# Performance work log

Measured on AMD Instinct MI355X. Metric: run time of the kernel, lower is better.

## Reference

```python
import jax, jax.numpy as jnp
import numpy as np

D_MODEL = 1024
N_HEADS = 16
D_K = D_MODEL // N_HEADS  # 64
ROPE_BASE = 10000.0
MASK_FILL = -1e9


def _rope_cos_sin(seq_len, d_k, dtype):
    # inv_freq over even dims, freqs = outer(t, inv_freq): [S, d_k//2]
    inv_freq = 1.0 / (ROPE_BASE ** (jnp.arange(0, d_k, 2, dtype=jnp.float32) / d_k))
    freqs = jnp.arange(seq_len, dtype=jnp.float32)[:, None] * inv_freq[None, :]
    # broadcast to full d_k (rotate_half convention: same freq for x1 and x2 halves)
    cos = jnp.concatenate([jnp.cos(freqs), jnp.cos(freqs)], axis=-1).astype(dtype)
    sin = jnp.concatenate([jnp.sin(freqs), jnp.sin(freqs)], axis=-1).astype(dtype)
    return cos, sin  # each [S, d_k]


def _apply_rope(x, cos, sin):
    # x: [B, H, S, d_k]; rotate_half: (x1, x2) -> (-x2, x1)
    x1, x2 = jnp.split(x, 2, axis=-1)
    rot = jnp.concatenate([-x2, x1], axis=-1)
    return x * cos[None, None] + rot * sin[None, None]


def setup_inputs() -> dict:
    key = jax.random.key(0)
    kx, kqkv, ko = jax.random.split(key, 3)
    x = jax.random.normal(kx, (1, 4096, D_MODEL), dtype=jnp.float32)
    # nn.Linear weight shape [out, in]; y = x @ W.T
    s = 1.0 / np.sqrt(D_MODEL)
    W_qkv = jax.random.uniform(kqkv, (3 * D_MODEL, D_MODEL), jnp.float32, -s, s)
    W_o = jax.random.uniform(ko, (D_MODEL, D_MODEL), jnp.float32, -s, s)
    return {"x": x, "W_qkv": W_qkv, "W_o": W_o}


def reference(x, W_qkv, W_o):
    B, S, _ = x.shape
    qkv = jnp.einsum("bsd,ed->bse", x, W_qkv)  # [B, S, 3*d_model]
    Q, K, V = jnp.split(qkv, 3, axis=-1)
    # [B, S, H, d_k] -> [B, H, S, d_k]
    reshape = lambda t: t.reshape(B, S, N_HEADS, D_K).transpose(0, 2, 1, 3)
    Q, K, V = reshape(Q), reshape(K), reshape(V)
    cos, sin = _rope_cos_sin(S, D_K, x.dtype)
    Q = _apply_rope(Q, cos, sin)
    K = _apply_rope(K, cos, sin)
    scores = jnp.einsum("bhqd,bhkd->bhqk", Q, K) / jnp.sqrt(jnp.asarray(D_K, x.dtype))
    causal = jnp.tril(jnp.ones((S, S), dtype=bool))
    scores = jnp.where(causal[None, None], scores, jnp.asarray(MASK_FILL, x.dtype))
    attn = jax.nn.softmax(scores, axis=-1)  # dropout inactive at inference
    out = jnp.einsum("bhqk,bhkd->bhqd", attn, V)
    out = out.transpose(0, 2, 1, 3).reshape(B, S, D_MODEL)
    return jnp.einsum("bsd,ed->bse", out, W_o)
```

## Files before the change

kernel.cpp:

```cpp
#include <hip/hip_runtime.h>


typedef __attribute__((ext_vector_type(8)))  short  short8;
typedef __attribute__((ext_vector_type(4)))  float  f32x4;
typedef __attribute__((ext_vector_type(16))) float  f32x16;
typedef __attribute__((ext_vector_type(4)))  float  float4v;
typedef __attribute__((ext_vector_type(4)))  unsigned short ushort4v;
typedef __attribute__((ext_vector_type(4)))  unsigned int   uint4v;

#define S_LEN 4096
#define DMODEL 1024
#define NHEADS 16
#define DKH 64

#define QSCALE 0.18033688011112042f

__device__ __forceinline__ unsigned short f2bf(float f) {
  unsigned u = __builtin_bit_cast(unsigned, f);
  u += 0x7FFFu + ((u >> 16) & 1u);
  return (unsigned short)(u >> 16);
}
__device__ __forceinline__ float bf2f(unsigned short h) {
  return __builtin_bit_cast(float, ((unsigned)h) << 16);
}

#define GLDS16(gsrc, ldst)                                                   \
  __builtin_amdgcn_global_load_lds(                                          \
      (const __attribute__((address_space(1))) void*)(gsrc),                 \
      (__attribute__((address_space(3))) void*)(ldst), 16, 0, 0)

__global__ void cvt_bf16_all(const float* __restrict__ x,    unsigned short* __restrict__ xb,
                             const float* __restrict__ wq,   unsigned short* __restrict__ wqb,
                             const float* __restrict__ wo,   unsigned short* __restrict__ wob) {
  int i = blockIdx.x * blockDim.x + threadIdx.x;
  const float* src; unsigned short* dst; int off;
  if (i < 1048576)               { src = x;  dst = xb;  off = i; }
  else if (i < 1048576 + 786432) { src = wq; dst = wqb; off = i - 1048576; }
  else                           { src = wo; dst = wob; off = i - 1048576 - 786432; }
  float4v v = reinterpret_cast<const float4v*>(src)[off];
  ushort4v o;
  o[0] = f2bf(v[0]); o[1] = f2bf(v[1]); o[2] = f2bf(v[2]); o[3] = f2bf(v[3]);
  reinterpret_cast<ushort4v*>(dst)[off] = o;
}

__global__ void rope_table(float2* __restrict__ tab) {
  int id = blockIdx.x * blockDim.x + threadIdx.x;
  int s = id >> 5, i = id & 31;
  float inv = expf(-(float)(2 * i) * (9.2103403719761836f / 64.0f));
  float ang = (float)s * inv;
  float sn, cs;
  sincosf(ang, &sn, &cs);
  tab[id] = make_float2(cs, sn);
}

__global__ __launch_bounds__(256) void gemm_qkv(const unsigned short* __restrict__ A,
                                                const unsigned short* __restrict__ B,
                                                const float2* __restrict__ tab,
                                                unsigned short* __restrict__ Qr,
                                                unsigned short* __restrict__ Kr,
                                                unsigned short* __restrict__ vtmp) {
  const int K = 1024;
  __shared__ __align__(16) unsigned short As[128 * 32];
  __shared__ __align__(16) unsigned short Bs[128 * 32];

  const int tid = threadIdx.x;
  const int l = tid & 63, w = tid >> 6;
  const int wr = w >> 1, wc = w & 1;
  const int bm = blockIdx.y * 128, bn = blockIdx.x * 128;
  const int lr = l & 15, lk = (l >> 4) * 8;

  f32x4 acc[4][4] = {};

  const unsigned short* Ag0 = A + (size_t)(bm + (tid >> 2)) * K + (tid & 3) * 8;
  const unsigned short* Ag1 = A + (size_t)(bm + 64 + (tid >> 2)) * K + (tid & 3) * 8;
  const unsigned short* Bg0 = B + (size_t)(bn + (tid >> 2)) * K + (tid & 3) * 8;
  const unsigned short* Bg1 = B + (size_t)(bn + 64 + (tid >> 2)) * K + (tid & 3) * 8;
  unsigned short* Ad0 = As + tid * 8;
  unsigned short* Ad1 = As + (tid + 256) * 8;
  unsigned short* Bd0 = Bs + tid * 8;
  unsigned short* Bd1 = Bs + (tid + 256) * 8;

  const unsigned short* Afr = As + (wr * 64 + lr) * 32 + lk;
  const unsigned short* Bfr = Bs + (wc * 64 + lr) * 32 + lk;

  for (int k0 = 0; k0 < K; k0 += 32) {
    GLDS16(Ag0 + k0, Ad0);
    GLDS16(Ag1 + k0, Ad1);
    GLDS16(Bg0 + k0, Bd0);
    GLDS16(Bg1 + k0, Bd1);
    __syncthreads();

    short8 af[4], bfr[4];
#pragma unroll
    for (int mi = 0; mi < 4; mi++) af[mi]  = *(const short8*)(Afr + mi * 16 * 32);
#pragma unroll
    for (int ni = 0; ni < 4; ni++) bfr[ni] = *(const short8*)(Bfr + ni * 16 * 32);

#pragma unroll
    for (int mi = 0; mi < 4; mi++)
#pragma unroll
      for (int ni = 0; ni < 4; ni++)
        acc[mi][ni] = __builtin_amdgcn_mfma_f32_16x16x32_bf16(af[mi], bfr[ni],
                                                              acc[mi][ni], 0, 0, 0);
    __syncthreads();
  }

  const int row0 = bm + wr * 64 + (l >> 4) * 4;
  const int region = bn >> 10;
  if (region < 2) {
    const int base64 = (bn & 1023) + wc * 64;
    const int h = base64 >> 6;
    unsigned short* dst = region ? Kr : Qr;
    const float scale = region ? 1.0f : QSCALE;
    const size_t hb = (size_t)h * S_LEN * DKH;
#pragma unroll
    for (int mi = 0; mi < 4; mi++)
#pragma unroll
      for (int jj = 0; jj < 4; jj++) {
        const int s = row0 + mi * 16 + jj;
        const float2 cs0 = tab[s * 32 + lr];
        const float2 cs1 = tab[s * 32 + lr + 16];
        const float x1 = acc[mi][0][jj], x2 = acc[mi][2][jj];
        const float y1 = acc[mi][1][jj], y2 = acc[mi][3][jj];
        const float o0 = (x1 * cs0.x - x2 * cs0.y) * scale;
        const float o2 = (x2 * cs0.x + x1 * cs0.y) * scale;
        const float o1 = (y1 * cs1.x - y2 * cs1.y) * scale;
        const float o3 = (y2 * cs1.x + y1 * cs1.y) * scale;
        const size_t a = hb + (size_t)s * DKH + lr;
        dst[a]      = f2bf(o0);
        dst[a + 16] = f2bf(o1);
        dst[a + 32] = f2bf(o2);
        dst[a + 48] = f2bf(o3);
      }
  } else {
    const int col0 = (bn - 2048) + wc * 64 + lr;
#pragma unroll
    for (int mi = 0; mi < 4; mi++)
#pragma unroll
      for (int ni = 0; ni < 4; ni++)
#pragma unroll
        for (int jj = 0; jj < 4; jj++)
          vtmp[(size_t)(row0 + mi * 16 + jj) * 1024 + col0 + ni * 16] =
              f2bf(acc[mi][ni][jj]);
  }
}

__global__ __launch_bounds__(256) void gemm_lds_f32(const unsigned short* __restrict__ A,
                                                    const unsigned short* __restrict__ B,
                                                    float* __restrict__ Cp,
                                                    int M, int N, int K) {
  __shared__ __align__(16) unsigned short As[128 * 32];
  __shared__ __align__(16) unsigned short Bs[128 * 32];

  const int tid = threadIdx.x;
  const int l = tid & 63, w = tid >> 6;
  const int wr = w >> 1, wc = w & 1;
  const int bm = blockIdx.y * 128, bn = blockIdx.x * 128;
  const int lr = l & 15, lk = (l >> 4) * 8;

  f32x4 acc[4][4] = {};

  const unsigned short* Ag0 = A + (size_t)(bm + (tid >> 2)) * K + (tid & 3) * 8;
  const unsigned short* Ag1 = A + (size_t)(bm + 64 + (tid >> 2)) * K + (tid & 3) * 8;
  const unsigned short* Bg0 = B + (size_t)(bn + (tid >> 2)) * K + (tid & 3) * 8;
  const unsigned short* Bg1 = B + (size_t)(bn + 64 + (tid >> 2)) * K + (tid & 3) * 8;
  unsigned short* Ad0 = As + tid * 8;
  unsigned short* Ad1 = As + (tid + 256) * 8;
  unsigned short* Bd0 = Bs + tid * 8;
  unsigned short* Bd1 = Bs + (tid + 256) * 8;

  const unsigned short* Afr = As + (wr * 64 + lr) * 32 + lk;
  const unsigned short* Bfr = Bs + (wc * 64 + lr) * 32 + lk;

  for (int k0 = 0; k0 < K; k0 += 32) {
    GLDS16(Ag0 + k0, Ad0);
    GLDS16(Ag1 + k0, Ad1);
    GLDS16(Bg0 + k0, Bd0);
    GLDS16(Bg1 + k0, Bd1);
    __syncthreads();

    short8 af[4], bfr[4];
#pragma unroll
    for (int mi = 0; mi < 4; mi++) af[mi]  = *(const short8*)(Afr + mi * 16 * 32);
#pragma unroll
    for (int ni = 0; ni < 4; ni++) bfr[ni] = *(const short8*)(Bfr + ni * 16 * 32);

#pragma unroll
    for (int mi = 0; mi < 4; mi++)
#pragma unroll
      for (int ni = 0; ni < 4; ni++)
        acc[mi][ni] = __builtin_amdgcn_mfma_f32_16x16x32_bf16(af[mi], bfr[ni],
                                                              acc[mi][ni], 0, 0, 0);
    __syncthreads();
  }

  const int row0 = bm + wr * 64 + (l >> 4) * 4;
  const int col0 = bn + wc * 64 + lr;
#pragma unroll
  for (int mi = 0; mi < 4; mi++)
#pragma unroll
    for (int ni = 0; ni < 4; ni++)
#pragma unroll
      for (int j = 0; j < 4; j++)
        Cp[(size_t)(row0 + mi * 16 + j) * N + (col0 + ni * 16)] = acc[mi][ni][j];
}

__global__ __launch_bounds__(256) void v_transpose(const unsigned short* __restrict__ vtmp,
                                                   unsigned short* __restrict__ Vt) {
  __shared__ unsigned lds[64 * 65];
  const int t  = threadIdx.x;
  const int b  = blockIdx.x;
  const int h  = b >> 6;
  const int s0 = (b & 63) * 64;

  const int sl = t >> 2;
  const int cq = (t & 3) * 16;
  {
    const unsigned short* src = vtmp + (size_t)(s0 + sl) * 1024 + h * 64 + cq;
    short8 v0 = *(const short8*)(src);
    short8 v1 = *(const short8*)(src + 8);
#pragma unroll
    for (int jj = 0; jj < 8; jj++) {
      lds[sl * 65 + cq + jj]     = (unsigned short)v0[jj];
      lds[sl * 65 + cq + 8 + jj] = (unsigned short)v1[jj];
    }
  }
  __syncthreads();

  const int dl = t >> 2;
  const int sq = (t & 3) * 16;
  short8 o0, o1;
#pragma unroll
  for (int k = 0; k < 8; k++) {
    o0[k] = (short)(unsigned short)lds[(sq + k) * 65 + dl];
    o1[k] = (short)(unsigned short)lds[(sq + 8 + k) * 65 + dl];
  }
  unsigned short* dst = Vt + (size_t)(h * 64 + dl) * S_LEN + s0 + sq;
  *(short8*)(dst)     = o0;
  *(short8*)(dst + 8) = o1;
}

__global__ __launch_bounds__(256) void flash_attn_kernel(const unsigned short* __restrict__ Qr,
                                                         const unsigned short* __restrict__ Kr,
                                                         const unsigned short* __restrict__ Vt,
                                                         unsigned short* __restrict__ O) {
  __shared__ __align__(16) char smem[2][16384];

  const int tid = threadIdx.x;
  const int l  = tid & 63;
  const int w  = tid >> 6;
  const int r  = l & 31;
  const int hi = l >> 5;
  const int wsub = w >> 1;
  const int wpar = w & 1;

  const int bx    = blockIdx.x;
  const int xcd   = bx & 7;
  const int j     = bx >> 3;
  const int h     = xcd * 2 + (j & 1);
  const int jj    = 63 - (j >> 1);
  const int q0    = jj * 64;

  const unsigned short* Qh = Qr + (size_t)h * S_LEN * DKH;
  const unsigned short* Kh = Kr + (size_t)h * S_LEN * DKH;
  const unsigned short* Vh = Vt + (size_t)h * DKH * S_LEN;

  const int qtile_w = 2 * jj + wsub;
  const int qbase   = q0 + wsub * 32;

  const int srow = tid >> 3;
  const int scol = (((tid & 7) * 16) ^ ((srow & 7) << 4)) >> 1;
  const size_t kbase = (size_t)srow * DKH + scol;
  const size_t vbase = (size_t)srow * S_LEN + scol;

  const int sw      = (r & 7) << 4;
  const int kfbyte  = (wpar * 32 + r) * 128;
  const int vfbyte0 = r * 128;
  const int vfbyte1 = (r + 32) * 128;
  const int vcol    = wpar * 64 + hi * 16;

  short8 qf[4];
  {
    const unsigned short* qb = Qh + (size_t)(qbase + r) * 64 + hi * 8;
#pragma unroll
    for (int dc = 0; dc < 4; dc++) qf[dc] = *(const short8*)(qb + dc * 16);
  }

  f32x16 acc0 = {}, acc1 = {};
  float m = -1e30f, lsum = 0.0f;

  const int nwin = jj + 1;

#pragma unroll
  for (int i = 0; i < 2; i++) {
    GLDS16(Kh + kbase + (size_t)i * 32 * DKH,   smem[0] + i * 4096 + tid * 16);
    GLDS16(Vh + vbase + (size_t)i * 32 * S_LEN, smem[0] + 8192 + i * 4096 + tid * 16);
  }
  __syncthreads();

  int buf = 0;
  for (int it = 0; it < nwin; it++) {
    if (it + 1 < nwin) {
      char* sd = smem[buf ^ 1];
      const unsigned short* Kg = Kh + (size_t)(it + 1) * 64 * DKH;
      const unsigned short* Vg = Vh + (size_t)(it + 1) * 64;
#pragma unroll
      for (int i = 0; i < 2; i++) {
        GLDS16(Kg + kbase + (size_t)i * 32 * DKH,   sd + i * 4096 + tid * 16);
        GLDS16(Vg + vbase + (size_t)i * 32 * S_LEN, sd + 8192 + i * 4096 + tid * 16);
      }
    }

    const char* sm = smem[buf];
    const int c = 2 * it + wpar;
    if (c <= qtile_w) {
      short8 kf[4], vf[4];
#pragma unroll
      for (int dc = 0; dc < 4; dc++)
        kf[dc] = *(const short8*)(sm + kfbyte + ((dc * 32 + hi * 16) ^ sw));
#pragma unroll
      for (int kc = 0; kc < 2; kc++) {
        vf[kc]     = *(const short8*)(sm + 8192 + vfbyte0 + ((vcol + kc * 32) ^ sw));
        vf[2 + kc] = *(const short8*)(sm + 8192 + vfbyte1 + ((vcol + kc * 32) ^ sw));
      }

      f32x16 st = {};
      __builtin_amdgcn_s_setprio(1);
      st = __builtin_amdgcn_mfma_f32_32x32x16_bf16(kf[0], qf[0], st, 0, 0, 0);
      st = __builtin_amdgcn_mfma_f32_32x32x16_bf16(kf[1], qf[1], st, 0, 0, 0);
      st = __builtin_amdgcn_mfma_f32_32x32x16_bf16(kf[2], qf[2], st, 0, 0, 0);
      st = __builtin_amdgcn_mfma_f32_32x32x16_bf16(kf[3], qf[3], st, 0, 0, 0);
      __builtin_amdgcn_s_setprio(0);

      if (c == qtile_w) {
#pragma unroll
        for (int reg = 0; reg < 16; reg++) {
          const int koff = (reg & 3) + 8 * (reg >> 2) + 4 * hi;
          if (koff > r) st[reg] = -1e30f;
        }
      }

      float t0 = fmaxf(fmaxf(st[0],  st[1]),  st[2]);
      float t1 = fmaxf(fmaxf(st[3],  st[4]),  st[5]);
      float t2 = fmaxf(fmaxf(st[6],  st[7]),  st[8]);
      float t3 = fmaxf(fmaxf(st[9],  st[10]), st[11]);
      float t4 = fmaxf(fmaxf(st[12], st[13]), st[14]);
      float pm = fmaxf(fmaxf(fmaxf(t0, t1), fmaxf(t2, t3)), fmaxf(t4, st[15]));
      pm = fmaxf(pm, __shfl_xor(pm, 32));

      if (!__all(pm <= m + 8.0f)) {
        float mn  = fmaxf(m, pm);
        float scl = exp2f(m - mn);
        m = mn;
        lsum *= scl;
#pragma unroll
        for (int reg = 0; reg < 16; reg++) { acc0[reg] *= scl; acc1[reg] *= scl; }
      }

      float p[16];
#pragma unroll
      for (int reg = 0; reg < 16; reg++) p[reg] = exp2f(st[reg] - m);

      float s2[8];
#pragma unroll
      for (int i = 0; i < 8; i++) s2[i] = p[2 * i] + p[2 * i + 1];
#pragma unroll
      for (int i = 0; i < 4; i++) s2[i] = s2[i] + s2[i + 4];
      float rs = (s2[0] + s2[2]) + (s2[1] + s2[3]);
      rs += __shfl_xor(rs, 32);
      lsum += rs;

      unsigned wd[8];
#pragma unroll
      for (int i = 0; i < 8; i++) {
        asm("v_cvt_pk_bf16_f32 %0, %1, %2" : "=v"(wd[i]) : "v"(p[2 * i]), "v"(p[2 * i + 1]));
      }
      unsigned pw[8];
#pragma unroll
      for (int i = 0; i < 8; i++) pw[i] = __shfl_xor(wd[i], 32);

      uint4v u0, u1;
      u0[0] = hi ? pw[2] : wd[0];
      u0[1] = hi ? pw[3] : wd[1];
      u0[2] = hi ? wd[2] : pw[0];
      u0[3] = hi ? wd[3] : pw[1];
      u1[0] = hi ? pw[6] : wd[4];
      u1[1] = hi ? pw[7] : wd[5];
      u1[2] = hi ? wd[6] : pw[4];
      u1[3] = hi ? wd[7] : pw[5];
      short8 pa0 = __builtin_bit_cast(short8, u0);
      short8 pa1 = __builtin_bit_cast(short8, u1);

      __builtin_amdgcn_s_setprio(1);
      acc0 = __builtin_amdgcn_mfma_f32_32x32x16_bf16(vf[0], pa0, acc0, 0, 0, 0);
      acc0 = __builtin_amdgcn_mfma_f32_32x32x16_bf16(vf[1], pa1, acc0, 0, 0, 0);
      acc1 = __builtin_amdgcn_mfma_f32_32x32x16_bf16(vf[2], pa0, acc1, 0, 0, 0);
      acc1 = __builtin_amdgcn_mfma_f32_32x32x16_bf16(vf[3], pa1, acc1, 0, 0, 0);
      __builtin_amdgcn_s_setprio(0);
    }

    __syncthreads();
    buf ^= 1;
  }

  unsigned (*oaccp)[32][33] = (unsigned (*)[32][33])smem;
  float* mlm = (float*)((char*)smem + 16896);
  float* mll = (float*)((char*)smem + 17408);

  if (hi == 0) { mlm[w * 32 + r] = m; mll[w * 32 + r] = lsum; }
#pragma unroll
  for (int i = 0; i < 8; i++) {
    const int widx = 4 * (i >> 1) + 2 * hi + (i & 1);
    unsigned ua, ub;
    asm("v_cvt_pk_bf16_f32 %0, %1, %2" : "=v"(ua) : "v"(acc0[2 * i]), "v"(acc0[2 * i + 1]));
    asm("v_cvt_pk_bf16_f32 %0, %1, %2" : "=v"(ub) : "v"(acc1[2 * i]), "v"(acc1[2 * i + 1]));
    oaccp[w][r][widx]      = ua;
    oaccp[w][r][16 + widx] = ub;
  }
  __syncthreads();

  const int st  = tid >> 7;
  const int rem = tid & 127;
  const int q   = rem >> 2;
  const int c0  = (rem & 3) * 8;
  const int w0  = 2 * st, w1 = 2 * st + 1;

  const float m0 = mlm[w0 * 32 + q], m1 = mlm[w1 * 32 + q];
  const float mmax = fmaxf(m0, m1);
  const float sc0 = exp2f(m0 - mmax), sc1 = exp2f(m1 - mmax);
  const float ltot = sc0 * mll[w0 * 32 + q] + sc1 * mll[w1 * 32 + q];
  const float rinv = 1.0f / ltot;

  float vs[16];
#pragma unroll
  for (int i = 0; i < 8; i++) {
    unsigned ua = oaccp[w0][q][c0 + i];
    unsigned ub = oaccp[w1][q][c0 + i];
    vs[2 * i]     = sc0 * __builtin_bit_cast(float, ua << 16)
                  + sc1 * __builtin_bit_cast(float, ub << 16);
    vs[2 * i + 1] = sc0 * __builtin_bit_cast(float, ua & 0xFFFF0000u)
                  + sc1 * __builtin_bit_cast(float, ub & 0xFFFF0000u);
  }
  short8 ov0, ov1;
#pragma unroll
  for (int i = 0; i < 8; i++) {
    ov0[i] = (short)f2bf(vs[i] * rinv);
    ov1[i] = (short)f2bf(vs[8 + i] * rinv);
  }
  unsigned short* op = O + (size_t)(q0 + st * 32 + q) * DMODEL + h * 64 + c0 * 2;
  *(short8*)(op)     = ov0;
  *(short8*)(op + 8) = ov1;
}

extern "C" void kernel_launch(void* const* d_in, const int* in_sizes, int n_in,
                              void* d_out, int out_size, void* d_ws, size_t ws_size,
                              hipStream_t stream) {
  (void)in_sizes; (void)n_in; (void)out_size; (void)ws_size;
  const float* x    = (const float*)d_in[0];
  const float* Wqkv = (const float*)d_in[1];
  const float* Wo   = (const float*)d_in[2];
  float* out = (float*)d_out;

  char* ws = (char*)d_ws;
  const size_t MB = 1u << 20;
  unsigned short* x_bf    = (unsigned short*)(ws + 0 * MB);
  unsigned short* wqkv_bf = (unsigned short*)(ws + 8 * MB);
  unsigned short* wo_bf   = (unsigned short*)(ws + 14 * MB);
  unsigned short* vtmp    = (unsigned short*)(ws + 16 * MB);
  float2*         tab     = (float2*)(ws + 24 * MB);
  unsigned short* Qr      = (unsigned short*)(ws + 40 * MB);
  unsigned short* Kr      = (unsigned short*)(ws + 48 * MB);
  unsigned short* Vt      = (unsigned short*)(ws + 56 * MB);
  unsigned short* Obf     = (unsigned short*)(ws + 64 * MB);

  cvt_bf16_all<<<8192, 256, 0, stream>>>(x, x_bf, Wqkv, wqkv_bf, Wo, wo_bf);
  rope_table<<<512, 256, 0, stream>>>(tab);

  gemm_qkv<<<dim3(3072 / 128, 4096 / 128), 256, 0, stream>>>(x_bf, wqkv_bf, tab,
                                                             Qr, Kr, vtmp);
  v_transpose<<<1024, 256, 0, stream>>>(vtmp, Vt);

  flash_attn_kernel<<<1024, 256, 0, stream>>>(Qr, Kr, Vt, Obf);

  gemm_lds_f32<<<dim3(1024 / 128, 4096 / 128), 256, 0, stream>>>(Obf, wo_bf, out,
                                                                 4096, 1024, 1024);
}
```

Measured before the change: 177.6 us.

## Fuse rope table into convert, write V transposed from GEMM, pair causal tiles

Folds the RoPE cos/sin table computation into the bf16 conversion kernel and has the QKV GEMM epilogue write V directly in transposed [h][d][s] layout, removing two kernel launches and the vtmp round trip. The flash attention block mapping now pairs a short causal query tile with a long one (t and 127-t) in the same block, so per-block work is balanced. The transposed V stores are strided 8-byte writes, which may coalesce worse than the separate transpose kernel did, and the paired halves of a block now run different loop lengths inside the shared window loop.

Measured after the change: 211.8 us. +19.3%, slower.

```diff
diff --git a/kernel.cpp b/kernel.cpp
--- a/kernel.cpp
+++ b/kernel.cpp
@@ -29,28 +29,32 @@
       (const __attribute__((address_space(1))) void*)(gsrc),                 \
       (__attribute__((address_space(3))) void*)(ldst), 16, 0, 0)
 
+#define CVT_TOTAL (1048576 + 786432 + 262144)
 __global__ void cvt_bf16_all(const float* __restrict__ x,    unsigned short* __restrict__ xb,
                              const float* __restrict__ wq,   unsigned short* __restrict__ wqb,
-                             const float* __restrict__ wo,   unsigned short* __restrict__ wob) {
+                             const float* __restrict__ wo,   unsigned short* __restrict__ wob,
+                             float2* __restrict__ tab) {
   int i = blockIdx.x * blockDim.x + threadIdx.x;
-  const float* src; unsigned short* dst; int off;
-  if (i < 1048576)               { src = x;  dst = xb;  off = i; }
-  else if (i < 1048576 + 786432) { src = wq; dst = wqb; off = i - 1048576; }
-  else                           { src = wo; dst = wob; off = i - 1048576 - 786432; }
-  float4v v = reinterpret_cast<const float4v*>(src)[off];
-  ushort4v o;
-  o[0] = f2bf(v[0]); o[1] = f2bf(v[1]); o[2] = f2bf(v[2]); o[3] = f2bf(v[3]);
-  reinterpret_cast<ushort4v*>(dst)[off] = o;
-}
-
-__global__ void rope_table(float2* __restrict__ tab) {
-  int id = blockIdx.x * blockDim.x + threadIdx.x;
-  int s = id >> 5, i = id & 31;
-  float inv = expf(-(float)(2 * i) * (9.2103403719761836f / 64.0f));
-  float ang = (float)s * inv;
-  float sn, cs;
-  sincosf(ang, &sn, &cs);
-  tab[id] = make_float2(cs, sn);
+  if (i < CVT_TOTAL) {
+    const float* src; unsigned short* dst; int off;
+    if (i < 1048576)               { src = x;  dst = xb;  off = i; }
+    else if (i < 1048576 + 786432) { src = wq; dst = wqb; off = i - 1048576; }
+    else                           { src = wo; dst = wob; off = i - 1048576 - 786432; }
+    float4v v = reinterpret_cast<const float4v*>(src)[off];
+    ushort4v o;
+    o[0] = f2bf(v[0]); o[1] = f2bf(v[1]); o[2] = f2bf(v[2]); o[3] = f2bf(v[3]);
+    reinterpret_cast<ushort4v*>(dst)[off] = o;
+  } else {
+    int id = i - CVT_TOTAL;
+    if (id < S_LEN * 32) {
+      int s = id >> 5, fi = id & 31;
+      float inv = expf(-(float)(2 * fi) * (9.2103403719761836f / 64.0f));
+      float ang = (float)s * inv;
+      float sn, cs;
+      sincosf(ang, &sn, &cs);
+      tab[id] = make_float2(cs, sn);
+    }
+  }
 }
 
 __global__ __launch_bounds__(256) void gemm_qkv(const unsigned short* __restrict__ A,
@@ -58,7 +62,7 @@
                                                 const float2* __restrict__ tab,
                                                 unsigned short* __restrict__ Qr,
                                                 unsigned short* __restrict__ Kr,
-                                                unsigned short* __restrict__ vtmp) {
+                                                unsigned short* __restrict__ Vt) {
   const int K = 1024;
   __shared__ __align__(16) unsigned short As[128 * 32];
   __shared__ __align__(16) unsigned short Bs[128 * 32];
@@ -133,15 +137,23 @@
         dst[a + 48] = f2bf(o3);
       }
   } else {
-    const int col0 = (bn - 2048) + wc * 64 + lr;
-#pragma unroll
-    for (int mi = 0; mi < 4; mi++)
-#pragma unroll
-      for (int ni = 0; ni < 4; ni++)
-#pragma unroll
-        for (int jj = 0; jj < 4; jj++)
-          vtmp[(size_t)(row0 + mi * 16 + jj) * 1024 + col0 + ni * 16] =
-              f2bf(acc[mi][ni][jj]);
+    const int colh = (bn - 2048) + wc * 64;
+    const int h = colh >> 6;
+    unsigned short* base = Vt + (size_t)h * DKH * S_LEN;
+#pragma unroll
+    for (int mi = 0; mi < 4; mi++) {
+      const int s = row0 + mi * 16;
+#pragma unroll
+      for (int ni = 0; ni < 4; ni++) {
+        const int d = ni * 16 + lr;
+        ushort4v pk;
+        pk[0] = f2bf(acc[mi][ni][0]);
+        pk[1] = f2bf(acc[mi][ni][1]);
+        pk[2] = f2bf(acc[mi][ni][2]);
+        pk[3] = f2bf(acc[mi][ni][3]);
+        *(ushort4v*)(base + (size_t)d * S_LEN + s) = pk;
+      }
+    }
   }
 }
 
@@ -205,41 +217,6 @@
         Cp[(size_t)(row0 + mi * 16 + j) * N + (col0 + ni * 16)] = acc[mi][ni][j];
 }
 
-__global__ __launch_bounds__(256) void v_transpose(const unsigned short* __restrict__ vtmp,
-                                                   unsigned short* __restrict__ Vt) {
-  __shared__ unsigned lds[64 * 65];
-  const int t  = threadIdx.x;
-  const int b  = blockIdx.x;
-  const int h  = b >> 6;
-  const int s0 = (b & 63) * 64;
-
-  const int sl = t >> 2;
-  const int cq = (t & 3) * 16;
-  {
-    const unsigned short* src = vtmp + (size_t)(s0 + sl) * 1024 + h * 64 + cq;
-    short8 v0 = *(const short8*)(src);
-    short8 v1 = *(const short8*)(src + 8);
-#pragma unroll
-    for (int jj = 0; jj < 8; jj++) {
-      lds[sl * 65 + cq + jj]     = (unsigned short)v0[jj];
-      lds[sl * 65 + cq + 8 + jj] = (unsigned short)v1[jj];
-    }
-  }
-  __syncthreads();
-
-  const int dl = t >> 2;
-  const int sq = (t & 3) * 16;
-  short8 o0, o1;
-#pragma unroll
-  for (int k = 0; k < 8; k++) {
-    o0[k] = (short)(unsigned short)lds[(sq + k) * 65 + dl];
-    o1[k] = (short)(unsigned short)lds[(sq + 8 + k) * 65 + dl];
-  }
-  unsigned short* dst = Vt + (size_t)(h * 64 + dl) * S_LEN + s0 + sq;
-  *(short8*)(dst)     = o0;
-  *(short8*)(dst + 8) = o1;
-}
-
 __global__ __launch_bounds__(256) void flash_attn_kernel(const unsigned short* __restrict__ Qr,
                                                          const unsigned short* __restrict__ Kr,
                                                          const unsigned short* __restrict__ Vt,
@@ -254,19 +231,19 @@
   const int wsub = w >> 1;
   const int wpar = w & 1;
 
-  const int bx    = blockIdx.x;
-  const int xcd   = bx & 7;
-  const int j     = bx >> 3;
-  const int h     = xcd * 2 + (j & 1);
-  const int jj    = 63 - (j >> 1);
-  const int q0    = jj * 64;
+  const int bx  = blockIdx.x;
+  const int xcd = bx & 7;
+  const int j   = bx >> 3;
+  const int h   = xcd * 2 + (j & 1);
+  const int t   = j >> 1;
+
+  const int sub    = wsub ? (127 - t) : t;
+  const int qbase  = sub * 32;
+  const int qtile_w = sub;
 
   const unsigned short* Qh = Qr + (size_t)h * S_LEN * DKH;
   const unsigned short* Kh = Kr + (size_t)h * S_LEN * DKH;
   const unsigned short* Vh = Vt + (size_t)h * DKH * S_LEN;
-
-  const int qtile_w = 2 * jj + wsub;
-  const int qbase   = q0 + wsub * 32;
 
   const int srow = tid >> 3;
   const int scol = (((tid & 7) * 16) ^ ((srow & 7) << 4)) >> 1;
@@ -289,7 +266,7 @@
   f32x16 acc0 = {}, acc1 = {};
   float m = -1e30f, lsum = 0.0f;
 
-  const int nwin = jj + 1;
+  const int nwin = ((127 - t) >> 1) + 1;
 
 #pragma unroll
   for (int i = 0; i < 2; i++) {
@@ -424,6 +401,7 @@
   const int q   = rem >> 2;
   const int c0  = (rem & 3) * 8;
   const int w0  = 2 * st, w1 = 2 * st + 1;
+  const int qrow0 = 32 * (st ? (127 - t) : t);
 
   const float m0 = mlm[w0 * 32 + q], m1 = mlm[w1 * 32 + q];
   const float mmax = fmaxf(m0, m1);
@@ -447,7 +425,7 @@
     ov0[i] = (short)f2bf(vs[i] * rinv);
     ov1[i] = (short)f2bf(vs[8 + i] * rinv);
   }
-  unsigned short* op = O + (size_t)(q0 + st * 32 + q) * DMODEL + h * 64 + c0 * 2;
+  unsigned short* op = O + (size_t)(qrow0 + q) * DMODEL + h * 64 + c0 * 2;
   *(short8*)(op)     = ov0;
   *(short8*)(op + 8) = ov1;
 }
@@ -466,19 +444,17 @@
   unsigned short* x_bf    = (unsigned short*)(ws + 0 * MB);
   unsigned short* wqkv_bf = (unsigned short*)(ws + 8 * MB);
   unsigned short* wo_bf   = (unsigned short*)(ws + 14 * MB);
-  unsigned short* vtmp    = (unsigned short*)(ws + 16 * MB);
   float2*         tab     = (float2*)(ws + 24 * MB);
   unsigned short* Qr      = (unsigned short*)(ws + 40 * MB);
   unsigned short* Kr      = (unsigned short*)(ws + 48 * MB);
   unsigned short* Vt      = (unsigned short*)(ws + 56 * MB);
   unsigned short* Obf     = (unsigned short*)(ws + 64 * MB);
 
-  cvt_bf16_all<<<8192, 256, 0, stream>>>(x, x_bf, Wqkv, wqkv_bf, Wo, wo_bf);
-  rope_table<<<512, 256, 0, stream>>>(tab);
+  cvt_bf16_all<<<(CVT_TOTAL + 131072 + 255) / 256, 256, 0, stream>>>(
+      x, x_bf, Wqkv, wqkv_bf, Wo, wo_bf, tab);
 
   gemm_qkv<<<dim3(3072 / 128, 4096 / 128), 256, 0, stream>>>(x_bf, wqkv_bf, tab,
-                                                             Qr, Kr, vtmp);
-  v_transpose<<<1024, 256, 0, stream>>>(vtmp, Vt);
+                                                             Qr, Kr, Vt);
 
   flash_attn_kernel<<<1024, 256, 0, stream>>>(Qr, Kr, Vt, Obf);
 
```
